# Optimization experiments

Measured on AMD Instinct MI355X. Metric: run time of the kernel, lower is better.

## Reference

```python
import jax, jax.numpy as jnp
import numpy as np

K = 4  # Chebyshev order (init arg)


def setup_inputs() -> dict:
    key = jax.random.key(0)
    k1, k2, k3, k4, k5 = jax.random.split(key, 5)
    N, M, Fin, Fout, E = 4, 100000, 32, 64, 1600000
    x = jax.random.normal(k1, (N, M, Fin), dtype=jnp.float32)
    edge_vals = jax.random.normal(k2, (E,), dtype=jnp.float32) * 0.1
    W = jax.random.normal(k3, (Fin * K, Fout), dtype=jnp.float32) * 0.05
    edge_rows = jax.random.randint(k4, (E,), 0, M, dtype=jnp.int32)
    edge_cols = jax.random.randint(k5, (E,), 0, M, dtype=jnp.int32)
    return {"x": x, "edge_vals": edge_vals, "W": W,
            "edge_rows": edge_rows, "edge_cols": edge_cols}


def reference(x, edge_vals, W, edge_rows, edge_cols):
    # x: [N, M, Fin]; L given in COO form (rows, cols, vals), shape [M, M].
    N, M, Fin = x.shape

    # [M, Fin*N] column-major-per-vertex layout, as in the original
    xt = jnp.transpose(x, (1, 2, 0)).reshape(M, Fin * N)

    def Lhat_matmul(v):
        # rescaled Laplacian: L' = 2*L/lmax - I with lmax=2  =>  L' v = L v - v
        gathered = edge_vals[:, None] * v[edge_cols]          # [E, Fin*N]
        Lv = jax.ops.segment_sum(gathered, edge_rows, num_segments=M)
        return Lv - v

    # Chebyshev recursion: T0 = x, T1 = L'x, T_k = 2 L' T_{k-1} - T_{k-2}
    Ts = [xt, Lhat_matmul(xt)]
    for _ in range(K - 2):
        Ts.append(2.0 * Lhat_matmul(Ts[-1]) - Ts[-2])
    xs = jnp.stack(Ts)                                        # [K, M, Fin*N]

    xs = xs.reshape(K, M, Fin, N).transpose(3, 1, 2, 0)       # [N, M, Fin, K]
    xs = xs.reshape(N * M, Fin * K)
    out = xs @ W                                              # [N*M, Fout]
    return out.reshape(N, M, W.shape[1])
```

## Files before the change

### kernel.cpp

```cpp
#include <hip/hip_runtime.h>
#include <hip/hip_bf16.h>
#include <stdint.h>

#define N_DIM 4
#define FIN 32
#define FOUT 64
#define ROWLEN 128
#define NBLK 256
#define BMAX 512

typedef __attribute__((ext_vector_type(4))) float f32x4;
typedef __attribute__((ext_vector_type(8))) short bf16x8;

__device__ __forceinline__ ushort f32_to_bf16_rn(float f) {
  uint u = __float_as_uint(f);
  u += 0x7FFFu + ((u >> 16) & 1u);
  return (ushort)(u >> 16);
}
__device__ __forceinline__ float bf16_lo(uint p) { return __uint_as_float(p << 16); }
__device__ __forceinline__ float bf16_hi(uint p) { return __uint_as_float(p & 0xFFFF0000u); }

__global__ void transpose_kernel(const float* __restrict__ x,
                                 float* __restrict__ Tf,
                                 ushort* __restrict__ Tb0, int MF) {
  int i = blockIdx.x * blockDim.x + threadIdx.x;
  if (i >= MF) return;
  float4 v;
  v.x = x[i];
  v.y = x[(size_t)MF + i];
  v.z = x[(size_t)2 * MF + i];
  v.w = x[(size_t)3 * MF + i];
  reinterpret_cast<float4*>(Tf)[i] = v;
  ushort4 h;
  h.x = f32_to_bf16_rn(v.x);
  h.y = f32_to_bf16_rn(v.y);
  h.z = f32_to_bf16_rn(v.z);
  h.w = f32_to_bf16_rn(v.w);
  reinterpret_cast<ushort4*>(Tb0)[i] = h;
}

__global__ __launch_bounds__(256) void bcount_kernel(
    const int* __restrict__ rows, int* __restrict__ c, int E, int B, int ce) {
  __shared__ int hist[BMAX];
  int tid = threadIdx.x, blk = blockIdx.x;
  for (int b = tid; b < B; b += 256) hist[b] = 0;
  __syncthreads();
  int start = blk * ce;
  int end = min(E, start + ce);
  for (int e = start + tid; e < end; e += 256)
    atomicAdd(&hist[rows[e] >> 8], 1);
  __syncthreads();
  for (int b = tid; b < B; b += 256) c[b * NBLK + blk] = hist[b];
}

__global__ __launch_bounds__(256) void bscanA_kernel(
    int* __restrict__ c, int* __restrict__ btot) {
  __shared__ int wsum[4];
  int b = blockIdx.x, tid = threadIdx.x;
  int lane = tid & 63, wid = tid >> 6;
  int v = c[b * NBLK + tid];
  int s = v;
#pragma unroll
  for (int off = 1; off < 64; off <<= 1) {
    int u = __shfl_up(s, off);
    if (lane >= off) s += u;
  }
  if (lane == 63) wsum[wid] = s;
  __syncthreads();
  if (tid == 0) {
    int run = 0;
#pragma unroll
    for (int w = 0; w < 4; ++w) { int t = wsum[w]; wsum[w] = run; run += t; }
  }
  __syncthreads();
  int excl = wsum[wid] + s - v;
  c[b * NBLK + tid] = excl;
  if (tid == 255) btot[b] = excl + v;
}

__global__ __launch_bounds__(512) void bscanB_kernel(
    const int* __restrict__ btot, int* __restrict__ bucket_start,
    int* __restrict__ row_start, int B, int M, int E) {
  __shared__ int wsum[8];
  int tid = threadIdx.x, lane = tid & 63, wid = tid >> 6;
  int v = (tid < B) ? btot[tid] : 0;
  int s = v;
#pragma unroll
  for (int off = 1; off < 64; off <<= 1) {
    int u = __shfl_up(s, off);
    if (lane >= off) s += u;
  }
  if (lane == 63) wsum[wid] = s;
  __syncthreads();
  if (tid == 0) {
    int run = 0;
#pragma unroll
    for (int w = 0; w < 8; ++w) { int t = wsum[w]; wsum[w] = run; run += t; }
  }
  __syncthreads();
  int excl = wsum[wid] + s - v;
  if (tid < B) bucket_start[tid] = excl;
  if (tid == 0) { bucket_start[B] = E; row_start[M] = E; }
}

__global__ __launch_bounds__(256) void bscatter_kernel(
    const int* __restrict__ rows, const int* __restrict__ cols,
    const float* __restrict__ vals, const int* __restrict__ c,
    const int* __restrict__ bucket_start, int2* __restrict__ binned,
    int E, int B, int ce) {
  __shared__ int base[BMAX];
  __shared__ int lcur[BMAX];
  int tid = threadIdx.x, blk = blockIdx.x;
  for (int b = tid; b < B; b += 256) {
    base[b] = bucket_start[b] + c[b * NBLK + blk];
    lcur[b] = 0;
  }
  __syncthreads();
  int start = blk * ce;
  int end = min(E, start + ce);
  for (int e = start + tid; e < end; e += 256) {
    int r = rows[e];
    int b = r >> 8;
    int pos = atomicAdd(&lcur[b], 1);
    binned[base[b] + pos] =
        make_int2(cols[e] | ((r & 255) << 17), __float_as_int(vals[e]));
  }
}

__global__ __launch_bounds__(256) void bsort_kernel(
    const int2* __restrict__ binned, const int* __restrict__ bucket_start,
    int2* __restrict__ csr, int* __restrict__ row_start, int M) {
  __shared__ int hist[256];
  __shared__ int wsum[4];
  int b = blockIdx.x, tid = threadIdx.x;
  int base = bucket_start[b];
  int cnt = bucket_start[b + 1] - base;
  hist[tid] = 0;
  __syncthreads();
  for (int i = tid; i < cnt; i += 256)
    atomicAdd(&hist[((unsigned)binned[base + i].x) >> 17], 1);
  __syncthreads();
  int v = hist[tid];
  int lane = tid & 63, wid = tid >> 6;
  int s = v;
#pragma unroll
  for (int off = 1; off < 64; off <<= 1) {
    int u = __shfl_up(s, off);
    if (lane >= off) s += u;
  }
  if (lane == 63) wsum[wid] = s;
  __syncthreads();
  if (tid == 0) {
    int run = 0;
#pragma unroll
    for (int w = 0; w < 4; ++w) { int t = wsum[w]; wsum[w] = run; run += t; }
  }
  __syncthreads();
  int excl = wsum[wid] + s - v;
  int r = (b << 8) + tid;
  if (r < M) row_start[r] = base + excl;
  __syncthreads();
  hist[tid] = excl;
  __syncthreads();
  for (int i = tid; i < cnt; i += 256) {
    int2 en = binned[base + i];
    int rl = ((unsigned)en.x) >> 17;
    int p = atomicAdd(&hist[rl], 1);
    csr[base + p] = make_int2(en.x & 0x1FFFF, en.y);
  }
}

__global__ __launch_bounds__(256) void spmm_kernel(
    float* __restrict__ Tf, const uint* __restrict__ srcb,
    const uint* __restrict__ prevb, uint* __restrict__ dstb,
    const int* __restrict__ row_start, const int2* __restrict__ csr,
    int M, float alpha, float beta, float gamma, int write_f32) {
  int wid = __builtin_amdgcn_readfirstlane((int)threadIdx.x >> 6);
  int gw = blockIdx.x * 4 + wid;
  int lane = threadIdx.x & 63;
  if (gw >= M) return;
  int s = row_start[gw];
  int e = row_start[gw + 1];
  float ax = 0.f, ay = 0.f;
  int j = s;
  for (; j + 8 <= e; j += 8) {
#pragma unroll
    for (int u = 0; u < 8; ++u) {
      int2 cv = csr[j + u];
      uint p = srcb[(size_t)(unsigned)cv.x * 64 + lane];
      float v = __int_as_float(cv.y);
      ax += v * bf16_lo(p);
      ay += v * bf16_hi(p);
    }
  }
  for (; j < e; ++j) {
    int2 cv = csr[j];
    uint p = srcb[(size_t)(unsigned)cv.x * 64 + lane];
    float v = __int_as_float(cv.y);
    ax += v * bf16_lo(p);
    ay += v * bf16_hi(p);
  }
  float2 sv = reinterpret_cast<const float2*>(Tf)[(size_t)gw * 64 + lane];
  ax = alpha * ax + beta * sv.x;
  ay = alpha * ay + beta * sv.y;
  if (prevb) {
    uint pp = prevb[(size_t)gw * 64 + lane];
    ax += gamma * bf16_lo(pp);
    ay += gamma * bf16_hi(pp);
  }
  if (write_f32)
    reinterpret_cast<float2*>(Tf)[(size_t)gw * 64 + lane] = make_float2(ax, ay);
  dstb[(size_t)gw * 64 + lane] =
      (uint)f32_to_bf16_rn(ax) | ((uint)f32_to_bf16_rn(ay) << 16);
}

__global__ __launch_bounds__(256) void gemm_kernel(
    const ushort* __restrict__ Tb0, const ushort* __restrict__ Tb1,
    const ushort* __restrict__ Tb2, const ushort* __restrict__ Tb3,
    const float* __restrict__ W, float* __restrict__ out,
    int M, int nwaves) {
  int lane = threadIdx.x & 63;
  int gwave = blockIdx.x * 4 + ((int)threadIdx.x >> 6);
  int g = lane >> 4;
  int q = lane & 15;

  bf16x8 b[4][4];
#pragma unroll
  for (int t = 0; t < 4; ++t) {
#pragma unroll
    for (int ft = 0; ft < 4; ++ft) {
#pragma unroll
      for (int e = 0; e < 8; ++e) {
        float w = W[(t * 32 + g * 8 + e) * FOUT + ft * 16 + q];
        b[t][ft][e] = (short)f32_to_bf16_rn(w);
      }
    }
  }

  int NT = (M + 3) >> 2;
  for (int tile = gwave; tile < NT; tile += nwaves) {
    int m0 = tile * 4;
    int mA = m0 + (q >> 2);
    if (mA > M - 1) mA = M - 1;
    int n = q & 3;
    size_t abase = (size_t)mA * ROWLEN + n;

    f32x4 C0 = {0.f, 0.f, 0.f, 0.f};
    f32x4 C1 = C0, C2 = C0, C3 = C0;
#pragma unroll
    for (int t = 0; t < 4; ++t) {
      int kc = t * 4 + g;
      bf16x8 a;
#pragma unroll
      for (int e = 0; e < 8; ++e) {
        int colT = (2 * kc + (e >> 2)) * 4;
        const ushort* Tb = (e & 3) == 0 ? Tb0 : (e & 3) == 1 ? Tb1
                         : (e & 3) == 2 ? Tb2 : Tb3;
        a[e] = (short)Tb[abase + colT];
      }
      C0 = __builtin_amdgcn_mfma_f32_16x16x32_bf16(a, b[t][0], C0, 0, 0, 0);
      C1 = __builtin_amdgcn_mfma_f32_16x16x32_bf16(a, b[t][1], C1, 0, 0, 0);
      C2 = __builtin_amdgcn_mfma_f32_16x16x32_bf16(a, b[t][2], C2, 0, 0, 0);
      C3 = __builtin_amdgcn_mfma_f32_16x16x32_bf16(a, b[t][3], C3, 0, 0, 0);
    }
    int mS = m0 + g;
    if (mS < M) {
#pragma unroll
      for (int r = 0; r < 4; ++r) {
        size_t ob = ((size_t)r * M + mS) * FOUT + q;
        out[ob +  0] = C0[r];
        out[ob + 16] = C1[r];
        out[ob + 32] = C2[r];
        out[ob + 48] = C3[r];
      }
    }
  }
}

extern "C" void kernel_launch(void* const* d_in, const int* in_sizes, int n_in,
                              void* d_out, int out_size, void* d_ws, size_t ws_size,
                              hipStream_t stream) {
  const float* x         = (const float*)d_in[0];
  const float* edge_vals = (const float*)d_in[1];
  const float* W         = (const float*)d_in[2];
  const int* edge_rows   = (const int*)d_in[3];
  const int* edge_cols   = (const int*)d_in[4];
  float* out = (float*)d_out;

  int M = in_sizes[0] / (N_DIM * FIN);
  int E = in_sizes[1];
  int MF = M * FIN;
  int B = (M + 255) >> 8;
  int ce = (E + NBLK - 1) / NBLK;

  char* ws = (char*)d_ws;
  size_t rowf = (size_t)M * ROWLEN;
  float* Tf = (float*)ws;
  ushort* Tb0 = (ushort*)(ws + rowf * sizeof(float));
  ushort* Tb1 = Tb0 + rowf;
  ushort* Tb2 = Tb1 + rowf;
  ushort* Tb3 = Tb2 + rowf;
  int2* binned = (int2*)(Tb3 + rowf);
  int2* csr = binned + E;
  int* c = (int*)(csr + E);
  int* btot = c + (size_t)B * NBLK;
  int* bucket_start = btot + B;
  int* row_start = bucket_start + (B + 1);

  transpose_kernel<<<(MF + 255) / 256, 256, 0, stream>>>(x, Tf, Tb0, MF);
  bcount_kernel<<<NBLK, 256, 0, stream>>>(edge_rows, c, E, B, ce);
  bscanA_kernel<<<B, 256, 0, stream>>>(c, btot);
  bscanB_kernel<<<1, 512, 0, stream>>>(btot, bucket_start, row_start, B, M, E);
  bscatter_kernel<<<NBLK, 256, 0, stream>>>(edge_rows, edge_cols, edge_vals,
                                            c, bucket_start, binned, E, B, ce);
  bsort_kernel<<<B, 256, 0, stream>>>(binned, bucket_start, csr, row_start, M);

  int spmm_blocks = (M + 3) / 4;
  spmm_kernel<<<spmm_blocks, 256, 0, stream>>>(
      Tf, (const uint*)Tb0, nullptr, (uint*)Tb1, row_start, csr,
      M, 1.f, -1.f, 0.f, 1);
  spmm_kernel<<<spmm_blocks, 256, 0, stream>>>(
      Tf, (const uint*)Tb1, (const uint*)Tb0, (uint*)Tb2, row_start, csr,
      M, 2.f, -2.f, -1.f, 1);
  spmm_kernel<<<spmm_blocks, 256, 0, stream>>>(
      Tf, (const uint*)Tb2, (const uint*)Tb1, (uint*)Tb3, row_start, csr,
      M, 2.f, -2.f, -1.f, 0);

  int gemm_blocks = 1024;
  gemm_kernel<<<gemm_blocks, 256, 0, stream>>>(
      Tb0, Tb1, Tb2, Tb3, W, out, M, gemm_blocks * 4);
}
```

Baseline: 350.9 us.

## Drop fp32 Chebyshev shadow buffer and switch to n-major bf16 row layout

The fp32 copy of the current Chebyshev term is removed, and the -v term in each SpMM step now reads the bf16 source row instead, cutting global memory traffic in the transpose and SpMM passes. The bf16 row layout changes from feature-interleaved to batch-major contiguous features. This lets the transpose write 16-byte vectors and lets the GEMM load each A fragment with a single 16-byte load instead of eight scattered 2-byte loads, with the W index remapped to match. The cost is extra rounding error, because the subtraction now uses bf16-rounded values rather than fp32.

```diff
diff --git a/kernel.cpp b/kernel.cpp
--- a/kernel.cpp
+++ b/kernel.cpp
@@ -21,22 +21,22 @@
 __device__ __forceinline__ float bf16_hi(uint p) { return __uint_as_float(p & 0xFFFF0000u); }
 
 __global__ void transpose_kernel(const float* __restrict__ x,
-                                 float* __restrict__ Tf,
-                                 ushort* __restrict__ Tb0, int MF) {
+                                 ushort* __restrict__ Tb0, int M) {
   int i = blockIdx.x * blockDim.x + threadIdx.x;
-  if (i >= MF) return;
-  float4 v;
-  v.x = x[i];
-  v.y = x[(size_t)MF + i];
-  v.z = x[(size_t)2 * MF + i];
-  v.w = x[(size_t)3 * MF + i];
-  reinterpret_cast<float4*>(Tf)[i] = v;
-  ushort4 h;
-  h.x = f32_to_bf16_rn(v.x);
-  h.y = f32_to_bf16_rn(v.y);
-  h.z = f32_to_bf16_rn(v.z);
-  h.w = f32_to_bf16_rn(v.w);
-  reinterpret_cast<ushort4*>(Tb0)[i] = h;
+  if (i >= M * 16) return;
+  int m = i >> 4;
+  int n = (i >> 2) & 3;
+  int f8 = i & 3;
+  const float* src = x + ((size_t)n * M + m) * FIN + f8 * 8;
+  float4 v0 = *reinterpret_cast<const float4*>(src);
+  float4 v1 = *reinterpret_cast<const float4*>(src + 4);
+  ushort h[8];
+  h[0] = f32_to_bf16_rn(v0.x); h[1] = f32_to_bf16_rn(v0.y);
+  h[2] = f32_to_bf16_rn(v0.z); h[3] = f32_to_bf16_rn(v0.w);
+  h[4] = f32_to_bf16_rn(v1.x); h[5] = f32_to_bf16_rn(v1.y);
+  h[6] = f32_to_bf16_rn(v1.z); h[7] = f32_to_bf16_rn(v1.w);
+  *reinterpret_cast<uint4*>(Tb0 + (size_t)m * ROWLEN + n * 32 + f8 * 8) =
+      *reinterpret_cast<const uint4*>(h);
 }
 
 __global__ __launch_bounds__(256) void bcount_kernel(
@@ -171,10 +171,10 @@
 }
 
 __global__ __launch_bounds__(256) void spmm_kernel(
-    float* __restrict__ Tf, const uint* __restrict__ srcb,
-    const uint* __restrict__ prevb, uint* __restrict__ dstb,
+    const uint* __restrict__ srcb, const uint* __restrict__ prevb,
+    uint* __restrict__ dstb,
     const int* __restrict__ row_start, const int2* __restrict__ csr,
-    int M, float alpha, float beta, float gamma, int write_f32) {
+    int M, float alpha, float beta, float gamma) {
   int wid = __builtin_amdgcn_readfirstlane((int)threadIdx.x >> 6);
   int gw = blockIdx.x * 4 + wid;
   int lane = threadIdx.x & 63;
@@ -200,16 +200,14 @@
     ax += v * bf16_lo(p);
     ay += v * bf16_hi(p);
   }
-  float2 sv = reinterpret_cast<const float2*>(Tf)[(size_t)gw * 64 + lane];
-  ax = alpha * ax + beta * sv.x;
-  ay = alpha * ay + beta * sv.y;
+  uint sp = srcb[(size_t)gw * 64 + lane];
+  ax = alpha * ax + beta * bf16_lo(sp);
+  ay = alpha * ay + beta * bf16_hi(sp);
   if (prevb) {
     uint pp = prevb[(size_t)gw * 64 + lane];
     ax += gamma * bf16_lo(pp);
     ay += gamma * bf16_hi(pp);
   }
-  if (write_f32)
-    reinterpret_cast<float2*>(Tf)[(size_t)gw * 64 + lane] = make_float2(ax, ay);
   dstb[(size_t)gw * 64 + lane] =
       (uint)f32_to_bf16_rn(ax) | ((uint)f32_to_bf16_rn(ay) << 16);
 }
@@ -231,7 +229,7 @@
     for (int ft = 0; ft < 4; ++ft) {
 #pragma unroll
       for (int e = 0; e < 8; ++e) {
-        float w = W[(t * 32 + g * 8 + e) * FOUT + ft * 16 + q];
+        float w = W[((8 * g + e) * 4 + t) * FOUT + ft * 16 + q];
         b[t][ft][e] = (short)f32_to_bf16_rn(w);
       }
     }
@@ -243,21 +241,14 @@
     int mA = m0 + (q >> 2);
     if (mA > M - 1) mA = M - 1;
     int n = q & 3;
-    size_t abase = (size_t)mA * ROWLEN + n;
+    size_t abase = (size_t)mA * ROWLEN + n * 32 + g * 8;
 
     f32x4 C0 = {0.f, 0.f, 0.f, 0.f};
     f32x4 C1 = C0, C2 = C0, C3 = C0;
 #pragma unroll
     for (int t = 0; t < 4; ++t) {
-      int kc = t * 4 + g;
-      bf16x8 a;
-#pragma unroll
-      for (int e = 0; e < 8; ++e) {
-        int colT = (2 * kc + (e >> 2)) * 4;
-        const ushort* Tb = (e & 3) == 0 ? Tb0 : (e & 3) == 1 ? Tb1
-                         : (e & 3) == 2 ? Tb2 : Tb3;
-        a[e] = (short)Tb[abase + colT];
-      }
+      const ushort* Tb = t == 0 ? Tb0 : t == 1 ? Tb1 : t == 2 ? Tb2 : Tb3;
+      bf16x8 a = *reinterpret_cast<const bf16x8*>(Tb + abase);
       C0 = __builtin_amdgcn_mfma_f32_16x16x32_bf16(a, b[t][0], C0, 0, 0, 0);
       C1 = __builtin_amdgcn_mfma_f32_16x16x32_bf16(a, b[t][1], C1, 0, 0, 0);
       C2 = __builtin_amdgcn_mfma_f32_16x16x32_bf16(a, b[t][2], C2, 0, 0, 0);
@@ -289,14 +280,12 @@
 
   int M = in_sizes[0] / (N_DIM * FIN);
   int E = in_sizes[1];
-  int MF = M * FIN;
   int B = (M + 255) >> 8;
   int ce = (E + NBLK - 1) / NBLK;
 
   char* ws = (char*)d_ws;
   size_t rowf = (size_t)M * ROWLEN;
-  float* Tf = (float*)ws;
-  ushort* Tb0 = (ushort*)(ws + rowf * sizeof(float));
+  ushort* Tb0 = (ushort*)ws;
   ushort* Tb1 = Tb0 + rowf;
   ushort* Tb2 = Tb1 + rowf;
   ushort* Tb3 = Tb2 + rowf;
@@ -307,7 +296,7 @@
   int* bucket_start = btot + B;
   int* row_start = bucket_start + (B + 1);
 
-  transpose_kernel<<<(MF + 255) / 256, 256, 0, stream>>>(x, Tf, Tb0, MF);
+  transpose_kernel<<<(M * 16 + 255) / 256, 256, 0, stream>>>(x, Tb0, M);
   bcount_kernel<<<NBLK, 256, 0, stream>>>(edge_rows, c, E, B, ce);
   bscanA_kernel<<<B, 256, 0, stream>>>(c, btot);
   bscanB_kernel<<<1, 512, 0, stream>>>(btot, bucket_start, row_start, B, M, E);
@@ -317,14 +306,14 @@
 
   int spmm_blocks = (M + 3) / 4;
   spmm_kernel<<<spmm_blocks, 256, 0, stream>>>(
-      Tf, (const uint*)Tb0, nullptr, (uint*)Tb1, row_start, csr,
-      M, 1.f, -1.f, 0.f, 1);
+      (const uint*)Tb0, nullptr, (uint*)Tb1, row_start, csr,
+      M, 1.f, -1.f, 0.f);
   spmm_kernel<<<spmm_blocks, 256, 0, stream>>>(
-      Tf, (const uint*)Tb1, (const uint*)Tb0, (uint*)Tb2, row_start, csr,
-      M, 2.f, -2.f, -1.f, 1);
+      (const uint*)Tb1, (const uint*)Tb0, (uint*)Tb2, row_start, csr,
+      M, 2.f, -2.f, -1.f);
   spmm_kernel<<<spmm_blocks, 256, 0, stream>>>(
-      Tf, (const uint*)Tb2, (const uint*)Tb1, (uint*)Tb3, row_start, csr,
-      M, 2.f, -2.f, -1.f, 0);
+      (const uint*)Tb2, (const uint*)Tb1, (uint*)Tb3, row_start, csr,
+      M, 2.f, -2.f, -1.f);
 
   int gemm_blocks = 1024;
   gemm_kernel<<<gemm_blocks, 256, 0, stream>>>(
```

Result: faster. 316.9 us (-9.7%).
